# Kernel tuning notes

Hardware: AMD Instinct MI355X
Metric: run time of the kernel (lower is better)

## Reference

```python
import jax, jax.numpy as jnp
import numpy as np

B, N, NFEAT, NHID, NHEADS, NCLASS, K1 = 4, 2048, 256, 64, 4, 32, 256
ALPHA = 0.2      # leaky relu slope
NEG = -9e15      # mask value used by the torch impl


def setup_inputs() -> dict:
    key = jax.random.key(0)
    ks = jax.random.split(key, 16)
    s = 0.05
    return {
        "x": jax.random.normal(ks[0], (B, N, NFEAT), jnp.float32),
        "adj": jax.random.randint(ks[1], (B, N, N), 0, 2).astype(jnp.int32),
        "one_hop_idcs": jax.random.randint(ks[2], (B, K1), 0, N),
        # multi-head GAT layer params (stacked over heads)
        "W": jax.random.normal(ks[3], (NHEADS, NFEAT, NHID), jnp.float32) * s,
        "a1": jax.random.normal(ks[4], (NHEADS, NHID), jnp.float32) * s,  # a[:nhid]
        "a2": jax.random.normal(ks[5], (NHEADS, NHID), jnp.float32) * s,  # a[nhid:]
        # output GAT layer params
        "Wo": jax.random.normal(ks[6], (NHEADS * NHID, NCLASS), jnp.float32) * s,
        "ao1": jax.random.normal(ks[7], (NCLASS,), jnp.float32) * s,
        "ao2": jax.random.normal(ks[8], (NCLASS,), jnp.float32) * s,
        # classifier: Linear(32, nclass) -> PReLU(nclass) -> Linear(nclass, 2)
        "W1": jax.random.normal(ks[9], (NCLASS, NCLASS), jnp.float32) * s,
        "b1": jnp.zeros((NCLASS,), jnp.float32),
        "prelu_w": jnp.full((NCLASS,), 0.25, jnp.float32),
        "W2": jax.random.normal(ks[10], (NCLASS, 2), jnp.float32) * s,
        "b2": jnp.zeros((2,), jnp.float32),
    }


def _gat_heads(x, W, a1, a2, adj):
    """Dense multi-head GAT. e_ij = leakyrelu(a^T [Wh_i || Wh_j]) computed
    as broadcast of two rank-1 projections (no [N,N,2d] concat tensor)."""
    Wh = jnp.einsum('bnf,hfd->bhnd', x, W)                 # [B,H,N,d]
    f1 = jnp.einsum('bhnd,hd->bhn', Wh, a1)                # src term
    f2 = jnp.einsum('bhnd,hd->bhn', Wh, a2)                # dst term
    e = jax.nn.leaky_relu(f1[:, :, :, None] + f2[:, :, None, :], ALPHA)
    e = jnp.where(adj[:, None, :, :] > 0, e, NEG)
    attn = jax.nn.softmax(e, axis=-1)                      # [B,H,N,N]
    h = jnp.einsum('bhnm,bhmd->bhnd', attn, Wh)            # [B,H,N,d]
    h = jax.nn.elu(h)                                      # concat=True -> elu
    # concat heads: [B,N,H*d]
    return h.transpose(0, 2, 1, 3).reshape(x.shape[0], x.shape[1], -1)


def _gat_out(x, Wo, ao1, ao2, adj):
    Wh = x @ Wo                                            # [B,N,nclass]
    f1 = Wh @ ao1
    f2 = Wh @ ao2
    e = jax.nn.leaky_relu(f1[:, :, None] + f2[:, None, :], ALPHA)
    e = jnp.where(adj > 0, e, NEG)
    attn = jax.nn.softmax(e, axis=-1)
    return attn @ Wh                                       # concat=False -> no elu here


def reference(x, adj, one_hop_idcs, W, a1, a2, Wo, ao1, ao2,
              W1, b1, prelu_w, W2, b2):
    h = _gat_heads(x, W, a1, a2, adj)          # [B,N,H*nhid]
    h = jax.nn.elu(_gat_out(h, Wo, ao1, ao2, adj))  # [B,N,nclass]
    # vectorized per-batch gather (replaces python loop over b)
    ef = jnp.take_along_axis(h, one_hop_idcs[:, :, None], axis=1)  # [B,K1,nclass]
    ef = ef.reshape(-1, h.shape[-1])
    y = ef @ W1 + b1
    y = jnp.where(y > 0, y, prelu_w * y)       # PReLU(nclass)
    return y @ W2 + b2                         # [B*K1, 2]
```

## Files before the change

kernel.cpp:

```cpp
#include <hip/hip_runtime.h>
#include <hip/hip_bf16.h>
#include <stdint.h>
#include <math.h>

#define BB 4
#define NN 2048
#define NFEAT 256
#define NHID 64
#define NHEADS 4
#define NCLASS 32
#define KK1 256
#define ALPHA 0.2f
#define LOG2E 1.4426950408889634f

typedef _Float16 f16x8 __attribute__((ext_vector_type(8)));
typedef _Float16 f16x4 __attribute__((ext_vector_type(4)));
typedef _Float16 h16x2 __attribute__((ext_vector_type(2)));
typedef float f32x4 __attribute__((ext_vector_type(4)));

__device__ __forceinline__ f16x8 ld8(const _Float16* p){
  f16x8 r;
  *(f16x4*)&r = *(const f16x4*)p;
  *((f16x4*)&r + 1) = *(const f16x4*)(p + 4);
  return r;
}

__device__ __forceinline__ h16x2 pk2(float a, float b){
  auto v = __builtin_amdgcn_cvt_pkrtz(a, b);
  h16x2 r;
  __builtin_memcpy(&r, &v, sizeof(r));
  return r;
}

__global__ void __launch_bounds__(256) pack_adj(const int* __restrict__ adj,
                                                unsigned long long* __restrict__ bits,
                                                int* __restrict__ cnt){
  __shared__ int csum[4];
  int row = blockIdx.x;
  const int* arow = adj + (size_t)row * NN;
  int lane = threadIdx.x & 63, wv = threadIdx.x >> 6;
  int c = 0;
  #pragma unroll
  for (int it=0; it<NN/256; ++it){
    int j = it*256 + threadIdx.x;
    unsigned long long m = __ballot(arow[j] > 0);
    if (lane==0){ bits[(size_t)row*(NN/64) + it*4 + wv] = m; c += __popcll(m); }
  }
  if (lane==0) csum[wv] = c;
  __syncthreads();
  if (threadIdx.x==0) cnt[row] = csum[0]+csum[1]+csum[2]+csum[3];
}

__global__ void __launch_bounds__(256) wh_proj2(const float* __restrict__ x,
        const float* __restrict__ W, const float* __restrict__ a1, const float* __restrict__ a2,
        _Float16* __restrict__ whT, float* __restrict__ f1l, float* __restrict__ f2l){
  __shared__ __align__(16) float xs[64*65];
  __shared__ float red1[4][64];
  __shared__ float red2[4][64];
  int bh = blockIdx.x >> 5;
  int i0 = (blockIdx.x & 31) * 64;
  int b = bh >> 2, h = bh & 3;
  int tid = threadIdx.x;
  int lane = tid & 63;
  int dbase = __builtin_amdgcn_readfirstlane(tid >> 6) * 16;
  float acc[16];
  #pragma unroll
  for (int dd=0; dd<16; ++dd) acc[dd] = 0.f;
  for (int kc=0; kc<4; ++kc){
    int kb = kc*64;
    __syncthreads();
    #pragma unroll
    for (int t=0; t<4; ++t){
      int row = t*16 + (tid>>4);
      int f4 = (tid&15)*4;
      float4 v = *(const float4*)(x + ((size_t)(b*NN + i0 + row))*NFEAT + kb + f4);
      xs[row*65 + f4 + 0] = v.x;
      xs[row*65 + f4 + 1] = v.y;
      xs[row*65 + f4 + 2] = v.z;
      xs[row*65 + f4 + 3] = v.w;
    }
    __syncthreads();
    const float* Wb = W + (size_t)h*NFEAT*NHID + (size_t)kb*NHID + dbase;
    #pragma unroll 4
    for (int f=0; f<64; ++f){
      float xv = xs[lane*65 + f];
      const float* wr = Wb + f*NHID;
      #pragma unroll
      for (int dd=0; dd<16; ++dd) acc[dd] = fmaf(xv, wr[dd], acc[dd]);
    }
  }
  float p1 = 0.f, p2 = 0.f;
  #pragma unroll
  for (int dd=0; dd<16; ++dd){
    int d = dbase + dd;
    whT[((size_t)bh*NHID + d)*NN + i0 + lane] = (_Float16)acc[dd];
    p1 = fmaf(acc[dd], a1[h*NHID + d], p1);
    p2 = fmaf(acc[dd], a2[h*NHID + d], p2);
  }
  int wv = tid >> 6;
  red1[wv][lane] = p1;
  red2[wv][lane] = p2;
  __syncthreads();
  if (tid < 64){
    float s1 = red1[0][tid]+red1[1][tid]+red1[2][tid]+red1[3][tid];
    float s2 = red2[0][tid]+red2[1][tid]+red2[2][tid]+red2[3][tid];
    f1l[(size_t)bh*NN + i0 + tid] = s1 * LOG2E;
    f2l[(size_t)bh*NN + i0 + tid] = s2 * LOG2E;
  }
}

__global__ void __launch_bounds__(256) attn_l1(
        const unsigned long long* __restrict__ bits,
        const _Float16* __restrict__ whT,
        const float* __restrict__ f1l, const float* __restrict__ f2l,
        const int* __restrict__ cnt_in,
        float* __restrict__ dst){
  const int JC = 128, PITCH = 132;
  __shared__ __align__(16) _Float16 whs[64*PITCH];
  __shared__ __align__(16) _Float16 wts[32*PITCH];
  __shared__ float ils[32];
  int tile = blockIdx.x & 63;
  int bh = blockIdx.x >> 6;
  int b = bh >> 2, h = bh & 3;
  int i0 = tile*32;
  int tid = threadIdx.x;
  int lane = tid & 63, wv = tid >> 6;
  int q = lane >> 4, col = lane & 15;
  int r = tid >> 3, jg = (tid & 7) * 16;
  float f1r = f1l[(size_t)bh*NN + i0 + r];
  bool czr = (cnt_in[b*NN + i0 + r] == 0);
  const unsigned short* mrow = (const unsigned short*)(bits + ((size_t)(b*NN + i0 + r))*(NN/64));
  const float* f2p = f2l + (size_t)bh*NN;
  const _Float16* whg = whT + (size_t)bh*NHID*NN;
  float lacc = 0.f;
  f32x4 c0 = {0.f,0.f,0.f,0.f}, c1 = {0.f,0.f,0.f,0.f};
  for (int it=0; it<NN/JC; ++it){
    __syncthreads();
    #pragma unroll
    for (int dd=0; dd<4; ++dd){
      int d = (tid>>4) + dd*16;
      int j8 = (tid&15)*8;
      uint4 v = *(const uint4*)(whg + (size_t)d*NN + it*JC + j8);
      uint2* w2 = (uint2*)&whs[d*PITCH + j8];
      w2[0] = uint2{v.x, v.y};
      w2[1] = uint2{v.z, v.w};
    }
    {
      unsigned int m16 = mrow[it*8 + (tid&7)];
      const float* fp = f2p + it*JC + jg;
      float4 fa = *(const float4*)(fp);
      float4 fb = *(const float4*)(fp+4);
      float4 fc = *(const float4*)(fp+8);
      float4 fd = *(const float4*)(fp+12);
      float fv[16] = {fa.x,fa.y,fa.z,fa.w, fb.x,fb.y,fb.z,fb.w,
                      fc.x,fc.y,fc.z,fc.w, fd.x,fd.y,fd.z,fd.w};
      h16x2 wp[8];
      #pragma unroll
      for (int p=0; p<8; ++p){
        float s0 = f1r + fv[2*p];
        float s1 = f1r + fv[2*p+1];
        s0 = (m16 & (1u<<(2*p)))   ? s0 : -1e5f;
        s1 = (m16 & (1u<<(2*p+1))) ? s1 : -1e5f;
        float e0 = fmaxf(s0, ALPHA*s0);
        float e1 = fmaxf(s1, ALPHA*s1);
        float w0 = exp2f(e0);
        float w1 = exp2f(e1);
        lacc += w0 + w1;
        wp[p] = pk2(w0, w1);
      }
      if (__builtin_expect(czr, 0)){
        h16x2 one2 = {(_Float16)1.f, (_Float16)1.f};
        #pragma unroll
        for (int p=0; p<8; ++p) wp[p] = one2;
      }
      uint2* wdst = (uint2*)&wts[r*PITCH + jg];
      const uint2* wsrc = (const uint2*)&wp[0];
      wdst[0]=wsrc[0]; wdst[1]=wsrc[1]; wdst[2]=wsrc[2]; wdst[3]=wsrc[3];
    }
    __syncthreads();
    #pragma unroll
    for (int ks=0; ks<4; ++ks){
      int kb = ks*32 + q*8;
      f16x8 a0 = ld8(&wts[col*PITCH + kb]);
      f16x8 a1v = ld8(&wts[(16+col)*PITCH + kb]);
      f16x8 bv = ld8(&whs[(wv*16+col)*PITCH + kb]);
      c0 = __builtin_amdgcn_mfma_f32_16x16x32_f16(a0, bv, c0, 0, 0, 0);
      c1 = __builtin_amdgcn_mfma_f32_16x16x32_f16(a1v, bv, c1, 0, 0, 0);
    }
  }
  lacc += __shfl_xor(lacc, 1, 64);
  lacc += __shfl_xor(lacc, 2, 64);
  lacc += __shfl_xor(lacc, 4, 64);
  if ((tid & 7) == 0) ils[r] = czr ? (1.0f/(float)NN) : 1.0f/lacc;
  __syncthreads();
  int dloc = wv*16 + col;
  #pragma unroll
  for (int mt=0; mt<2; ++mt){
    #pragma unroll
    for (int reg=0; reg<4; ++reg){
      int ir = mt*16 + q*4 + reg;
      float v = (mt==0 ? c0[reg] : c1[reg]) * ils[ir];
      v = v > 0.f ? v : expm1f(v);
      dst[((size_t)(b*NN + i0 + ir))*(NHEADS*NHID) + h*NHID + dloc] = v;
    }
  }
}

__global__ void __launch_bounds__(256) out_proj2(const float* __restrict__ h1,
        const float* __restrict__ Wo, const float* __restrict__ ao1, const float* __restrict__ ao2,
        _Float16* __restrict__ whT2, float* __restrict__ f1ol, float* __restrict__ f2ol){
  __shared__ __align__(16) float xs[64*65];
  __shared__ float red1[4][64];
  __shared__ float red2[4][64];
  int b = blockIdx.x >> 5;
  int i0 = (blockIdx.x & 31) * 64;
  int tid = threadIdx.x;
  int lane = tid & 63;
  int dbase = __builtin_amdgcn_readfirstlane(tid >> 6) * 8;
  float acc[8];
  #pragma unroll
  for (int dd=0; dd<8; ++dd) acc[dd] = 0.f;
  for (int kc=0; kc<4; ++kc){
    int kb = kc*64;
    __syncthreads();
    #pragma unroll
    for (int t=0; t<4; ++t){
      int row = t*16 + (tid>>4);
      int f4 = (tid&15)*4;
      float4 v = *(const float4*)(h1 + ((size_t)(b*NN + i0 + row))*256 + kb + f4);
      xs[row*65 + f4 + 0] = v.x;
      xs[row*65 + f4 + 1] = v.y;
      xs[row*65 + f4 + 2] = v.z;
      xs[row*65 + f4 + 3] = v.w;
    }
    __syncthreads();
    #pragma unroll 4
    for (int f=0; f<64; ++f){
      float xv = xs[lane*65 + f];
      const float* wr = Wo + (size_t)(kb+f)*NCLASS + dbase;
      #pragma unroll
      for (int dd=0; dd<8; ++dd) acc[dd] = fmaf(xv, wr[dd], acc[dd]);
    }
  }
  float p1 = 0.f, p2 = 0.f;
  #pragma unroll
  for (int dd=0; dd<8; ++dd){
    int d = dbase + dd;
    whT2[((size_t)b*NCLASS + d)*NN + i0 + lane] = (_Float16)acc[dd];
    p1 = fmaf(acc[dd], ao1[d], p1);
    p2 = fmaf(acc[dd], ao2[d], p2);
  }
  int wv = tid >> 6;
  red1[wv][lane] = p1;
  red2[wv][lane] = p2;
  __syncthreads();
  if (tid < 64){
    float s1 = red1[0][tid]+red1[1][tid]+red1[2][tid]+red1[3][tid];
    float s2 = red2[0][tid]+red2[1][tid]+red2[2][tid]+red2[3][tid];
    f1ol[(size_t)b*NN + i0 + tid] = s1 * LOG2E;
    f2ol[(size_t)b*NN + i0 + tid] = s2 * LOG2E;
  }
}

__global__ void __launch_bounds__(256) attn_l2(
        const unsigned long long* __restrict__ bits,
        const _Float16* __restrict__ whT2,
        const float* __restrict__ f1ol, const float* __restrict__ f2ol,
        const int* __restrict__ cnt_in, const int* __restrict__ oh,
        float* __restrict__ pc, float* __restrict__ pl){
  const int JC = 128, PITCH = 132;
  __shared__ __align__(16) _Float16 whs[32*PITCH];
  __shared__ __align__(16) _Float16 wts[32*PITCH];
  int blk = blockIdx.x;
  int js = blk & 7, kt = (blk>>3) & 7, b = blk >> 6;
  int tid = threadIdx.x;
  int lane = tid & 63, wv = tid >> 6;
  int q = lane >> 4, col = lane & 15;
  int r = tid >> 3, jg = (tid & 7) * 16;
  int row_i = oh[b*KK1 + kt*32 + r];
  float f1r = f1ol[b*NN + row_i];
  bool czr = (cnt_in[b*NN + row_i] == 0);
  const unsigned short* mrow = (const unsigned short*)(bits + ((size_t)(b*NN + row_i))*(NN/64));
  const float* f2p = f2ol + (size_t)b*NN;
  const _Float16* whg = whT2 + (size_t)b*NCLASS*NN;
  float lacc = 0.f;
  f32x4 c0 = {0.f,0.f,0.f,0.f};
  int mt = wv & 1, nt = wv >> 1;
  for (int ii=0; ii<2; ++ii){
    int it = js*2 + ii;
    __syncthreads();
    #pragma unroll
    for (int dd=0; dd<2; ++dd){
      int d = (tid>>4) + dd*16;
      int j8 = (tid&15)*8;
      uint4 v = *(const uint4*)(whg + (size_t)d*NN + it*JC + j8);
      uint2* w2 = (uint2*)&whs[d*PITCH + j8];
      w2[0] = uint2{v.x, v.y};
      w2[1] = uint2{v.z, v.w};
    }
    {
      unsigned int m16 = mrow[it*8 + (tid&7)];
      const float* fp = f2p + it*JC + jg;
      float4 fa = *(const float4*)(fp);
      float4 fb = *(const float4*)(fp+4);
      float4 fc = *(const float4*)(fp+8);
      float4 fd = *(const float4*)(fp+12);
      float fv[16] = {fa.x,fa.y,fa.z,fa.w, fb.x,fb.y,fb.z,fb.w,
                      fc.x,fc.y,fc.z,fc.w, fd.x,fd.y,fd.z,fd.w};
      h16x2 wp[8];
      #pragma unroll
      for (int p=0; p<8; ++p){
        float s0 = f1r + fv[2*p];
        float s1 = f1r + fv[2*p+1];
        s0 = (m16 & (1u<<(2*p)))   ? s0 : -1e5f;
        s1 = (m16 & (1u<<(2*p+1))) ? s1 : -1e5f;
        float e0 = fmaxf(s0, ALPHA*s0);
        float e1 = fmaxf(s1, ALPHA*s1);
        float w0 = exp2f(e0);
        float w1 = exp2f(e1);
        lacc += w0 + w1;
        wp[p] = pk2(w0, w1);
      }
      if (__builtin_expect(czr, 0)){
        h16x2 one2 = {(_Float16)1.f, (_Float16)1.f};
        #pragma unroll
        for (int p=0; p<8; ++p) wp[p] = one2;
        lacc += 16.f;
      }
      uint2* wdst = (uint2*)&wts[r*PITCH + jg];
      const uint2* wsrc = (const uint2*)&wp[0];
      wdst[0]=wsrc[0]; wdst[1]=wsrc[1]; wdst[2]=wsrc[2]; wdst[3]=wsrc[3];
    }
    __syncthreads();
    #pragma unroll
    for (int ks=0; ks<4; ++ks){
      int kb = ks*32 + q*8;
      f16x8 a0 = ld8(&wts[(mt*16+col)*PITCH + kb]);
      f16x8 bv = ld8(&whs[(nt*16+col)*PITCH + kb]);
      c0 = __builtin_amdgcn_mfma_f32_16x16x32_f16(a0, bv, c0, 0, 0, 0);
    }
  }
  lacc += __shfl_xor(lacc, 1, 64);
  lacc += __shfl_xor(lacc, 2, 64);
  lacc += __shfl_xor(lacc, 4, 64);
  if ((tid & 7) == 0) pl[blk*32 + r] = lacc;
  int dloc = nt*16 + col;
  #pragma unroll
  for (int reg=0; reg<4; ++reg){
    int ir = mt*16 + q*4 + reg;
    pc[(size_t)blk*1024 + ir*32 + dloc] = c0[reg];
  }
}

__global__ void __launch_bounds__(256) classify2(const float* __restrict__ pc,
        const float* __restrict__ pl,
        const float* __restrict__ W1, const float* __restrict__ b1,
        const float* __restrict__ pw, const float* __restrict__ W2, const float* __restrict__ b2,
        float* __restrict__ out){
  __shared__ float efs[4][32];
  int wv = threadIdx.x >> 6;
  int lane = threadIdx.x & 63;
  int row = blockIdx.x*4 + wv;
  int b = row >> 8, k = row & 255;
  int kt = k >> 5, r = k & 31;
  int base = (b*8 + kt)*8;
  if (lane < 32){
    float s = 0.f, l = 0.f;
    #pragma unroll
    for (int js=0; js<8; ++js){
      s += pc[(size_t)(base+js)*1024 + r*32 + lane];
      l += pl[(base+js)*32 + r];
    }
    float v = s / l;
    v = v > 0.f ? v : expm1f(v);
    efs[wv][lane] = v;
  }
  __syncthreads();
  const float* ef = efs[wv];
  int c = lane & 31;
  float y = b1[c];
  #pragma unroll 8
  for (int kk=0; kk<32; ++kk) y += ef[kk] * W1[kk*32 + c];
  y = y > 0.f ? y : pw[c]*y;
  float o0 = y * W2[c*2+0];
  float o1 = y * W2[c*2+1];
  #pragma unroll
  for (int o=16;o>0;o>>=1){ o0 += __shfl_xor(o0,o,64); o1 += __shfl_xor(o1,o,64); }
  if (lane==0){ out[row*2+0] = o0 + b2[0]; out[row*2+1] = o1 + b2[1]; }
}

extern "C" void kernel_launch(void* const* d_in, const int* in_sizes, int n_in,
                              void* d_out, int out_size, void* d_ws, size_t ws_size,
                              hipStream_t stream) {
  const float* x    = (const float*)d_in[0];
  const int*   adj  = (const int*)  d_in[1];
  const int*   oh   = (const int*)  d_in[2];
  const float* W    = (const float*)d_in[3];
  const float* a1   = (const float*)d_in[4];
  const float* a2   = (const float*)d_in[5];
  const float* Wo   = (const float*)d_in[6];
  const float* ao1  = (const float*)d_in[7];
  const float* ao2  = (const float*)d_in[8];
  const float* W1   = (const float*)d_in[9];
  const float* b1   = (const float*)d_in[10];
  const float* pw   = (const float*)d_in[11];
  const float* W2   = (const float*)d_in[12];
  const float* b2   = (const float*)d_in[13];
  float* out = (float*)d_out;

  char* base = (char*)d_ws;
  size_t off = 0;
  auto alloc = [&](size_t bytes)->char*{
    char* p = base + off;
    off = (off + bytes + 255) & ~(size_t)255;
    return p;
  };
  unsigned long long* adjbits = (unsigned long long*)alloc((size_t)BB*NN*(NN/64)*8);
  int*   cnt1 = (int*)  alloc((size_t)BB*NN*4);
  _Float16* WhT  = (_Float16*)alloc((size_t)BB*NHEADS*NHID*NN*2);
  float* f1l  = (float*)alloc((size_t)BB*NHEADS*NN*4);
  float* f2l  = (float*)alloc((size_t)BB*NHEADS*NN*4);
  float* h1   = (float*)alloc((size_t)BB*NN*(NHEADS*NHID)*4);
  _Float16* WhT2 = (_Float16*)alloc((size_t)BB*NCLASS*NN*2);
  float* f1ol = (float*)alloc((size_t)BB*NN*4);
  float* f2ol = (float*)alloc((size_t)BB*NN*4);
  float* pc   = (float*)alloc((size_t)256*1024*4);
  float* pl   = (float*)alloc((size_t)256*32*4);

  pack_adj<<<BB*NN, 256, 0, stream>>>(adj, adjbits, cnt1);
  wh_proj2<<<BB*NHEADS*(NN/64), 256, 0, stream>>>(x, W, a1, a2, WhT, f1l, f2l);
  attn_l1<<<BB*NHEADS*(NN/32), 256, 0, stream>>>(adjbits, WhT, f1l, f2l, cnt1, h1);
  out_proj2<<<BB*(NN/64), 256, 0, stream>>>(h1, Wo, ao1, ao2, WhT2, f1ol, f2ol);
  attn_l2<<<BB*8*8, 256, 0, stream>>>(adjbits, WhT2, f1ol, f2ol, cnt1, oh, pc, pl);
  classify2<<<(BB*KK1)/4, 256, 0, stream>>>(pc, pl, W1, b1, pw, W2, b2, out);
}
```

Before: 223.7 us.

## Split attention K-dimension across waves, load operands directly into MFMA registers

The layer-1 attention kernel no longer stages weights and Wh tiles through shared memory with per-iteration barriers. Each wave now owns a quarter of the neighbor dimension, computes its own attention weights straight into MFMA A-fragments and loads Wh B-fragments from global memory. Partial accumulators and row sums are reduced across waves through shared memory once at the end. Separately, exp2f is replaced with the raw hardware exp2 intrinsic in both attention kernels. The trade-off is redundant global loads of Wh per wave, more accumulator registers, and a final cross-wave reduction, in exchange for removing the barrier-bound staging loop.

```diff
diff --git a/kernel.cpp b/kernel.cpp
--- a/kernel.cpp
+++ b/kernel.cpp
@@ -115,10 +115,9 @@
         const float* __restrict__ f1l, const float* __restrict__ f2l,
         const int* __restrict__ cnt_in,
         float* __restrict__ dst){
-  const int JC = 128, PITCH = 132;
-  __shared__ __align__(16) _Float16 whs[64*PITCH];
-  __shared__ __align__(16) _Float16 wts[32*PITCH];
-  __shared__ float ils[32];
+  const int CP = 68;
+  __shared__ __align__(16) float cred[4][32*CP];
+  __shared__ float lred[4][32];
   int tile = blockIdx.x & 63;
   int bh = blockIdx.x >> 6;
   int b = bh >> 2, h = bh & 3;
@@ -126,84 +125,90 @@
   int tid = threadIdx.x;
   int lane = tid & 63, wv = tid >> 6;
   int q = lane >> 4, col = lane & 15;
-  int r = tid >> 3, jg = (tid & 7) * 16;
-  float f1r = f1l[(size_t)bh*NN + i0 + r];
-  bool czr = (cnt_in[b*NN + i0 + r] == 0);
-  const unsigned short* mrow = (const unsigned short*)(bits + ((size_t)(b*NN + i0 + r))*(NN/64));
+  int r0 = i0 + col, r1 = i0 + 16 + col;
+  float f1a = f1l[(size_t)bh*NN + r0];
+  float f1b = f1l[(size_t)bh*NN + r1];
+  bool cza = (cnt_in[b*NN + r0] == 0);
+  bool czb = (cnt_in[b*NN + r1] == 0);
+  const unsigned int* ma = (const unsigned int*)(bits + ((size_t)(b*NN + r0))*(NN/64));
+  const unsigned int* mb = (const unsigned int*)(bits + ((size_t)(b*NN + r1))*(NN/64));
   const float* f2p = f2l + (size_t)bh*NN;
   const _Float16* whg = whT + (size_t)bh*NHID*NN;
-  float lacc = 0.f;
-  f32x4 c0 = {0.f,0.f,0.f,0.f}, c1 = {0.f,0.f,0.f,0.f};
-  for (int it=0; it<NN/JC; ++it){
-    __syncthreads();
-    #pragma unroll
-    for (int dd=0; dd<4; ++dd){
-      int d = (tid>>4) + dd*16;
-      int j8 = (tid&15)*8;
-      uint4 v = *(const uint4*)(whg + (size_t)d*NN + it*JC + j8);
-      uint2* w2 = (uint2*)&whs[d*PITCH + j8];
-      w2[0] = uint2{v.x, v.y};
-      w2[1] = uint2{v.z, v.w};
-    }
-    {
-      unsigned int m16 = mrow[it*8 + (tid&7)];
-      const float* fp = f2p + it*JC + jg;
-      float4 fa = *(const float4*)(fp);
-      float4 fb = *(const float4*)(fp+4);
-      float4 fc = *(const float4*)(fp+8);
-      float4 fd = *(const float4*)(fp+12);
-      float fv[16] = {fa.x,fa.y,fa.z,fa.w, fb.x,fb.y,fb.z,fb.w,
-                      fc.x,fc.y,fc.z,fc.w, fd.x,fd.y,fd.z,fd.w};
-      h16x2 wp[8];
+  float la = 0.f, lb = 0.f;
+  f32x4 acc[2][4];
+  #pragma unroll
+  for (int mt=0; mt<2; ++mt)
+    #pragma unroll
+    for (int nt=0; nt<4; ++nt) acc[mt][nt] = f32x4{0.f,0.f,0.f,0.f};
+
+  #pragma unroll 2
+  for (int ks=0; ks<16; ++ks){
+    int jb = wv*512 + ks*32;
+    int j8 = jb + q*8;
+    unsigned int mwa = ma[jb>>5];
+    unsigned int mwb = mb[jb>>5];
+    float4 fa  = *(const float4*)(f2p + j8);
+    float4 fbv = *(const float4*)(f2p + j8 + 4);
+    float fvv[8] = {fa.x,fa.y,fa.z,fa.w, fbv.x,fbv.y,fbv.z,fbv.w};
+    union { f16x8 v; h16x2 h[4]; } ua, ub;
+    #pragma unroll
+    for (int p=0; p<4; ++p){
+      unsigned sh = q*8 + 2*p;
+      float s00 = f1a + fvv[2*p],   s01 = f1a + fvv[2*p+1];
+      float s10 = f1b + fvv[2*p],   s11 = f1b + fvv[2*p+1];
+      s00 = ((mwa>>sh)&1u)     ? s00 : -1e5f;
+      s01 = ((mwa>>(sh+1))&1u) ? s01 : -1e5f;
+      s10 = ((mwb>>sh)&1u)     ? s10 : -1e5f;
+      s11 = ((mwb>>(sh+1))&1u) ? s11 : -1e5f;
+      float w00 = __builtin_amdgcn_exp2f(fmaxf(s00, ALPHA*s00));
+      float w01 = __builtin_amdgcn_exp2f(fmaxf(s01, ALPHA*s01));
+      float w10 = __builtin_amdgcn_exp2f(fmaxf(s10, ALPHA*s10));
+      float w11 = __builtin_amdgcn_exp2f(fmaxf(s11, ALPHA*s11));
+      w00 = cza ? 1.f : w00;  w01 = cza ? 1.f : w01;
+      w10 = czb ? 1.f : w10;  w11 = czb ? 1.f : w11;
+      la += w00 + w01;  lb += w10 + w11;
+      ua.h[p] = pk2(w00, w01);
+      ub.h[p] = pk2(w10, w11);
+    }
+    #pragma unroll
+    for (int nt=0; nt<4; ++nt){
+      f16x8 bv = ld8(whg + (size_t)(nt*16 + col)*NN + j8);
+      acc[0][nt] = __builtin_amdgcn_mfma_f32_16x16x32_f16(ua.v, bv, acc[0][nt], 0, 0, 0);
+      acc[1][nt] = __builtin_amdgcn_mfma_f32_16x16x32_f16(ub.v, bv, acc[1][nt], 0, 0, 0);
+    }
+  }
+  la += __shfl_xor(la, 16, 64);  la += __shfl_xor(la, 32, 64);
+  lb += __shfl_xor(lb, 16, 64);  lb += __shfl_xor(lb, 32, 64);
+  if (q == 0){ lred[wv][col] = la; lred[wv][16+col] = lb; }
+  #pragma unroll
+  for (int mt=0; mt<2; ++mt)
+    #pragma unroll
+    for (int nt=0; nt<4; ++nt)
       #pragma unroll
-      for (int p=0; p<8; ++p){
-        float s0 = f1r + fv[2*p];
-        float s1 = f1r + fv[2*p+1];
-        s0 = (m16 & (1u<<(2*p)))   ? s0 : -1e5f;
-        s1 = (m16 & (1u<<(2*p+1))) ? s1 : -1e5f;
-        float e0 = fmaxf(s0, ALPHA*s0);
-        float e1 = fmaxf(s1, ALPHA*s1);
-        float w0 = exp2f(e0);
-        float w1 = exp2f(e1);
-        lacc += w0 + w1;
-        wp[p] = pk2(w0, w1);
-      }
-      if (__builtin_expect(czr, 0)){
-        h16x2 one2 = {(_Float16)1.f, (_Float16)1.f};
-        #pragma unroll
-        for (int p=0; p<8; ++p) wp[p] = one2;
-      }
-      uint2* wdst = (uint2*)&wts[r*PITCH + jg];
-      const uint2* wsrc = (const uint2*)&wp[0];
-      wdst[0]=wsrc[0]; wdst[1]=wsrc[1]; wdst[2]=wsrc[2]; wdst[3]=wsrc[3];
-    }
-    __syncthreads();
-    #pragma unroll
-    for (int ks=0; ks<4; ++ks){
-      int kb = ks*32 + q*8;
-      f16x8 a0 = ld8(&wts[col*PITCH + kb]);
-      f16x8 a1v = ld8(&wts[(16+col)*PITCH + kb]);
-      f16x8 bv = ld8(&whs[(wv*16+col)*PITCH + kb]);
-      c0 = __builtin_amdgcn_mfma_f32_16x16x32_f16(a0, bv, c0, 0, 0, 0);
-      c1 = __builtin_amdgcn_mfma_f32_16x16x32_f16(a1v, bv, c1, 0, 0, 0);
-    }
-  }
-  lacc += __shfl_xor(lacc, 1, 64);
-  lacc += __shfl_xor(lacc, 2, 64);
-  lacc += __shfl_xor(lacc, 4, 64);
-  if ((tid & 7) == 0) ils[r] = czr ? (1.0f/(float)NN) : 1.0f/lacc;
+      for (int reg=0; reg<4; ++reg)
+        cred[wv][(mt*16 + q*4 + reg)*CP + nt*16 + col] = acc[mt][nt][reg];
   __syncthreads();
-  int dloc = wv*16 + col;
-  #pragma unroll
-  for (int mt=0; mt<2; ++mt){
-    #pragma unroll
-    for (int reg=0; reg<4; ++reg){
-      int ir = mt*16 + q*4 + reg;
-      float v = (mt==0 ? c0[reg] : c1[reg]) * ils[ir];
-      v = v > 0.f ? v : expm1f(v);
-      dst[((size_t)(b*NN + i0 + ir))*(NHEADS*NHID) + h*NHID + dloc] = v;
-    }
-  }
+  int row = tid >> 3, d0 = (tid & 7) * 8;
+  float l = lred[0][row] + lred[1][row] + lred[2][row] + lred[3][row];
+  bool cz = (cnt_in[b*NN + i0 + row] == 0);
+  float il = cz ? (1.0f/(float)NN) : 1.0f/l;
+  float4 s0 = {0,0,0,0}, s1 = {0,0,0,0};
+  #pragma unroll
+  for (int w=0; w<4; ++w){
+    float4 v0 = *(const float4*)&cred[w][row*CP + d0];
+    float4 v1 = *(const float4*)&cred[w][row*CP + d0 + 4];
+    s0.x+=v0.x; s0.y+=v0.y; s0.z+=v0.z; s0.w+=v0.w;
+    s1.x+=v1.x; s1.y+=v1.y; s1.z+=v1.z; s1.w+=v1.w;
+  }
+  float ov[8] = {s0.x,s0.y,s0.z,s0.w, s1.x,s1.y,s1.z,s1.w};
+  #pragma unroll
+  for (int dd=0; dd<8; ++dd){
+    float v = ov[dd]*il;
+    ov[dd] = v > 0.f ? v : expm1f(v);
+  }
+  float* dp = dst + ((size_t)(b*NN + i0 + row))*(NHEADS*NHID) + h*NHID + d0;
+  *(float4*)dp       = float4{ov[0],ov[1],ov[2],ov[3]};
+  *(float4*)(dp + 4) = float4{ov[4],ov[5],ov[6],ov[7]};
 }
 
 __global__ void __launch_bounds__(256) out_proj2(const float* __restrict__ h1,
@@ -316,8 +321,8 @@
         s1 = (m16 & (1u<<(2*p+1))) ? s1 : -1e5f;
         float e0 = fmaxf(s0, ALPHA*s0);
         float e1 = fmaxf(s1, ALPHA*s1);
-        float w0 = exp2f(e0);
-        float w1 = exp2f(e1);
+        float w0 = __builtin_amdgcn_exp2f(e0);
+        float w1 = __builtin_amdgcn_exp2f(e1);
         lacc += w0 + w1;
         wp[p] = pk2(w0, w1);
       }
```

Result: slower. 250.2 us (+11.9%).

## Compute attention weights in MFMA A-fragment registers and widen row tile to 64

Applied to the files above, without the earlier changes.

The layer-1 attention kernel now gives each wave 16 query rows and all 64 output dims. Each lane computes its masked exp weights directly in the layout the MFMA A operand needs, so the shared-memory staging buffer for weights and one barrier per iteration go away. The row tile doubles to 64, which halves the block count and the redundant loads of Wh per row. The raw hardware exp2 intrinsic replaces exp2f in both attention kernels. The trade-offs are more accumulator registers per thread, fewer blocks in flight, and exp work done in 4 waves that each redo the f2 loads.

```diff
diff --git a/kernel.cpp b/kernel.cpp
--- a/kernel.cpp
+++ b/kernel.cpp
@@ -115,93 +115,87 @@
         const float* __restrict__ f1l, const float* __restrict__ f2l,
         const int* __restrict__ cnt_in,
         float* __restrict__ dst){
-  const int JC = 128, PITCH = 132;
+  const int PITCH = 136;
   __shared__ __align__(16) _Float16 whs[64*PITCH];
-  __shared__ __align__(16) _Float16 wts[32*PITCH];
-  __shared__ float ils[32];
-  int tile = blockIdx.x & 63;
-  int bh = blockIdx.x >> 6;
+  __shared__ float ils[4][16];
+  int tile = blockIdx.x & 31;
+  int bh = blockIdx.x >> 5;
   int b = bh >> 2, h = bh & 3;
-  int i0 = tile*32;
+  int i0 = tile*64;
   int tid = threadIdx.x;
-  int lane = tid & 63, wv = tid >> 6;
+  int lane = tid & 63, w = tid >> 6;
   int q = lane >> 4, col = lane & 15;
-  int r = tid >> 3, jg = (tid & 7) * 16;
-  float f1r = f1l[(size_t)bh*NN + i0 + r];
-  bool czr = (cnt_in[b*NN + i0 + r] == 0);
-  const unsigned short* mrow = (const unsigned short*)(bits + ((size_t)(b*NN + i0 + r))*(NN/64));
+  int mrow = i0 + w*16 + col;
+  float f1r = f1l[(size_t)bh*NN + mrow];
+  bool cz = (cnt_in[b*NN + mrow] == 0);
+  const unsigned int* mr = (const unsigned int*)(bits + ((size_t)(b*NN + mrow))*(NN/64));
   const float* f2p = f2l + (size_t)bh*NN;
   const _Float16* whg = whT + (size_t)bh*NHID*NN;
+  int sd = tid >> 2, sq = tid & 3;
+  const _Float16* sg = whg + (size_t)sd*NN + sq*32;
+  _Float16* sl = whs + sd*PITCH + sq*32;
   float lacc = 0.f;
-  f32x4 c0 = {0.f,0.f,0.f,0.f}, c1 = {0.f,0.f,0.f,0.f};
-  for (int it=0; it<NN/JC; ++it){
-    __syncthreads();
-    #pragma unroll
-    for (int dd=0; dd<4; ++dd){
-      int d = (tid>>4) + dd*16;
-      int j8 = (tid&15)*8;
-      uint4 v = *(const uint4*)(whg + (size_t)d*NN + it*JC + j8);
-      uint2* w2 = (uint2*)&whs[d*PITCH + j8];
-      w2[0] = uint2{v.x, v.y};
-      w2[1] = uint2{v.z, v.w};
-    }
+  f32x4 acc[4];
+  #pragma unroll
+  for (int nt=0; nt<4; ++nt) acc[nt] = f32x4{0.f,0.f,0.f,0.f};
+
+  for (int it=0; it<16; ++it){
+    __syncthreads();
     {
-      unsigned int m16 = mrow[it*8 + (tid&7)];
-      const float* fp = f2p + it*JC + jg;
-      float4 fa = *(const float4*)(fp);
-      float4 fb = *(const float4*)(fp+4);
-      float4 fc = *(const float4*)(fp+8);
-      float4 fd = *(const float4*)(fp+12);
-      float fv[16] = {fa.x,fa.y,fa.z,fa.w, fb.x,fb.y,fb.z,fb.w,
-                      fc.x,fc.y,fc.z,fc.w, fd.x,fd.y,fd.z,fd.w};
-      h16x2 wp[8];
+      uint4 t0 = *(const uint4*)(sg + it*128);
+      uint4 t1 = *(const uint4*)(sg + it*128 + 8);
+      uint4 t2 = *(const uint4*)(sg + it*128 + 16);
+      uint4 t3 = *(const uint4*)(sg + it*128 + 24);
+      *(uint4*)(sl)      = t0;
+      *(uint4*)(sl + 8)  = t1;
+      *(uint4*)(sl + 16) = t2;
+      *(uint4*)(sl + 24) = t3;
+    }
+    uint4 mw4 = *(const uint4*)(mr + it*4);
+    __syncthreads();
+    #pragma unroll
+    for (int ks=0; ks<4; ++ks){
+      unsigned int mw = ((const unsigned int*)&mw4)[ks];
+      int j8 = it*128 + ks*32 + q*8;
+      float4 fa = *(const float4*)(f2p + j8);
+      float4 fb = *(const float4*)(f2p + j8 + 4);
+      float fv[8] = {fa.x,fa.y,fa.z,fa.w, fb.x,fb.y,fb.z,fb.w};
+      union { f16x8 v; h16x2 h[4]; } ua;
       #pragma unroll
-      for (int p=0; p<8; ++p){
+      for (int p=0; p<4; ++p){
+        unsigned sh = q*8 + 2*p;
         float s0 = f1r + fv[2*p];
         float s1 = f1r + fv[2*p+1];
-        s0 = (m16 & (1u<<(2*p)))   ? s0 : -1e5f;
-        s1 = (m16 & (1u<<(2*p+1))) ? s1 : -1e5f;
-        float e0 = fmaxf(s0, ALPHA*s0);
-        float e1 = fmaxf(s1, ALPHA*s1);
-        float w0 = exp2f(e0);
-        float w1 = exp2f(e1);
+        s0 = ((mw>>sh)&1u)     ? s0 : -1e5f;
+        s1 = ((mw>>(sh+1))&1u) ? s1 : -1e5f;
+        float w0 = __builtin_amdgcn_exp2f(fmaxf(s0, ALPHA*s0));
+        float w1 = __builtin_amdgcn_exp2f(fmaxf(s1, ALPHA*s1));
+        w0 = cz ? 1.f : w0;
+        w1 = cz ? 1.f : w1;
         lacc += w0 + w1;
-        wp[p] = pk2(w0, w1);
+        ua.h[p] = pk2(w0, w1);
       }
-      if (__builtin_expect(czr, 0)){
-        h16x2 one2 = {(_Float16)1.f, (_Float16)1.f};
-        #pragma unroll
-        for (int p=0; p<8; ++p) wp[p] = one2;
+      #pragma unroll
+      for (int nt=0; nt<4; ++nt){
+        f16x8 bv = ld8(&whs[(nt*16 + col)*PITCH + ks*32 + q*8]);
+        acc[nt] = __builtin_amdgcn_mfma_f32_16x16x32_f16(ua.v, bv, acc[nt], 0, 0, 0);
       }
-      uint2* wdst = (uint2*)&wts[r*PITCH + jg];
-      const uint2* wsrc = (const uint2*)&wp[0];
-      wdst[0]=wsrc[0]; wdst[1]=wsrc[1]; wdst[2]=wsrc[2]; wdst[3]=wsrc[3];
-    }
-    __syncthreads();
-    #pragma unroll
-    for (int ks=0; ks<4; ++ks){
-      int kb = ks*32 + q*8;
-      f16x8 a0 = ld8(&wts[col*PITCH + kb]);
-      f16x8 a1v = ld8(&wts[(16+col)*PITCH + kb]);
-      f16x8 bv = ld8(&whs[(wv*16+col)*PITCH + kb]);
-      c0 = __builtin_amdgcn_mfma_f32_16x16x32_f16(a0, bv, c0, 0, 0, 0);
-      c1 = __builtin_amdgcn_mfma_f32_16x16x32_f16(a1v, bv, c1, 0, 0, 0);
-    }
-  }
-  lacc += __shfl_xor(lacc, 1, 64);
-  lacc += __shfl_xor(lacc, 2, 64);
-  lacc += __shfl_xor(lacc, 4, 64);
-  if ((tid & 7) == 0) ils[r] = czr ? (1.0f/(float)NN) : 1.0f/lacc;
+    }
+  }
+  lacc += __shfl_xor(lacc, 16, 64);
+  lacc += __shfl_xor(lacc, 32, 64);
+  if (q == 0) ils[w][col] = 1.0f / lacc;
   __syncthreads();
-  int dloc = wv*16 + col;
-  #pragma unroll
-  for (int mt=0; mt<2; ++mt){
-    #pragma unroll
-    for (int reg=0; reg<4; ++reg){
-      int ir = mt*16 + q*4 + reg;
-      float v = (mt==0 ? c0[reg] : c1[reg]) * ils[ir];
+  #pragma unroll
+  for (int reg=0; reg<4; ++reg){
+    int ir = q*4 + reg;
+    float ilv = ils[w][ir];
+    float* dp = dst + ((size_t)(b*NN + i0 + w*16 + ir))*(NHEADS*NHID) + h*NHID + col;
+    #pragma unroll
+    for (int nt=0; nt<4; ++nt){
+      float v = acc[nt][reg] * ilv;
       v = v > 0.f ? v : expm1f(v);
-      dst[((size_t)(b*NN + i0 + ir))*(NHEADS*NHID) + h*NHID + dloc] = v;
+      dp[nt*16] = v;
     }
   }
 }
@@ -316,8 +310,8 @@
         s1 = (m16 & (1u<<(2*p+1))) ? s1 : -1e5f;
         float e0 = fmaxf(s0, ALPHA*s0);
         float e1 = fmaxf(s1, ALPHA*s1);
-        float w0 = exp2f(e0);
-        float w1 = exp2f(e1);
+        float w0 = __builtin_amdgcn_exp2f(e0);
+        float w1 = __builtin_amdgcn_exp2f(e1);
         lacc += w0 + w1;
         wp[p] = pk2(w0, w1);
       }
@@ -429,7 +423,7 @@
 
   pack_adj<<<BB*NN, 256, 0, stream>>>(adj, adjbits, cnt1);
   wh_proj2<<<BB*NHEADS*(NN/64), 256, 0, stream>>>(x, W, a1, a2, WhT, f1l, f2l);
-  attn_l1<<<BB*NHEADS*(NN/32), 256, 0, stream>>>(adjbits, WhT, f1l, f2l, cnt1, h1);
+  attn_l1<<<BB*NHEADS*(NN/64), 256, 0, stream>>>(adjbits, WhT, f1l, f2l, cnt1, h1);
   out_proj2<<<BB*(NN/64), 256, 0, stream>>>(h1, Wo, ao1, ao2, WhT2, f1ol, f2ol);
   attn_l2<<<BB*8*8, 256, 0, stream>>>(adjbits, WhT2, f1ol, f2ol, cnt1, oh, pc, pl);
   classify2<<<(BB*KK1)/4, 256, 0, stream>>>(pc, pl, W1, b1, pw, W2, b2, out);
```

After: 235.0 us. +5.1%, slower.
